# Kernel tuning notes

Measured on AMD Instinct MI355X. Metric: run time of the kernel, lower is better.

Reference implementation:

```python
import jax, jax.numpy as jnp
import numpy as np

B, S, D, H = 4, 2048, 1024, 16
DK = D // H

def setup_inputs() -> dict:
    key = jax.random.key(0)
    ks = jax.random.split(key, 12)
    s = 1.0 / np.sqrt(D)
    return {
        "query": jax.random.normal(ks[0], (B, S, D), jnp.float32),
        "key": jax.random.normal(ks[1], (B, S, D), jnp.float32),
        "value": jax.random.normal(ks[2], (B, S, D), jnp.float32),
        "mask": jax.random.randint(ks[3], (B, S, S), 0, 2, jnp.int32),
        "Wq": jax.random.normal(ks[4], (D, D), jnp.float32) * s,
        "bq": jnp.zeros((D,), jnp.float32),
        "Wk": jax.random.normal(ks[5], (D, D), jnp.float32) * s,
        "bk": jnp.zeros((D,), jnp.float32),
        "Wv": jax.random.normal(ks[6], (D, D), jnp.float32) * s,
        "bv": jnp.zeros((D,), jnp.float32),
        "Wo": jax.random.normal(ks[7], (D, D), jnp.float32) * s,
        "bo": jnp.zeros((D,), jnp.float32),
    }

def _split_heads(x):
    b, s, _ = x.shape
    return x.reshape(b, s, H, DK).transpose(0, 2, 1, 3)  # [b,h,s,dk]

def reference(query, key, value, mask, Wq, bq, Wk, bk, Wv, bv, Wo, bo):
    # torch nn.Linear: y = x @ W.T + b
    Q = _split_heads(query @ Wq.T + bq)
    K = _split_heads(key @ Wk.T + bk)
    V = _split_heads(value @ Wv.T + bv)
    scores = jnp.einsum('bhqd,bhkd->bhqk', Q, K) / np.sqrt(DK)
    scores = jnp.where(mask[:, None, :, :] == 0, jnp.float32(-1e9), scores)
    probs = jax.nn.softmax(scores, axis=-1)
    attn = jnp.einsum('bhqk,bhkd->bhqd', probs, V)
    out = attn.transpose(0, 2, 1, 3).reshape(query.shape[0], -1, H * DK)
    return out @ Wo.T + bo
```

## Files before the change

kernel.cpp:

```cpp
#include <hip/hip_runtime.h>

typedef __attribute__((ext_vector_type(8))) short short8;
typedef __attribute__((ext_vector_type(8))) unsigned short ushort8_t;
typedef __attribute__((ext_vector_type(4))) float floatx4;
typedef __attribute__((ext_vector_type(2))) _Float16 half2_t;
typedef __attribute__((ext_vector_type(4))) _Float16 half4;
typedef __attribute__((ext_vector_type(8))) _Float16 half8;
typedef __attribute__((ext_vector_type(2))) unsigned int uint2v;

#define B_ 4
#define S_ 2048
#define D_ 1024
#define H_ 16
#define DK_ 64
#define BS_ (B_ * S_)

union V8u { half8 v8; half4 v4[2]; };
union H16 { _Float16 h; unsigned short u; };

typedef const __attribute__((address_space(1))) void* gvp;
typedef __attribute__((address_space(3))) void* lvp;

static __device__ __forceinline__ unsigned short f2bf(float f) {
  union { float f; unsigned int u; } x; x.f = f;
  unsigned int r = x.u + 0x7fffu + ((x.u >> 16) & 1u);
  return (unsigned short)(r >> 16);
}

static __device__ __forceinline__ half2_t pk_f16(float a, float b) {
  return __builtin_bit_cast(half2_t, __builtin_amdgcn_cvt_pkrtz(a, b));
}

static __device__ __forceinline__ float fexp2(float x) {
  float r;
  asm("v_exp_f32 %0, %1" : "=v"(r) : "v"(x));
  return r;
}

static __device__ __forceinline__ half8 mk8(uint2v a, uint2v b) {
  union { unsigned u[4]; half8 h; } t;
  t.u[0] = a.x; t.u[1] = a.y; t.u[2] = b.x; t.u[3] = b.y;
  return t.h;
}

__global__ void cast3_kernel(const float* __restrict__ a, const float* __restrict__ b,
                             const float* __restrict__ c,
                             unsigned short* __restrict__ oa, unsigned short* __restrict__ ob,
                             unsigned short* __restrict__ oc, int n4) {
  int i = blockIdx.x * blockDim.x + threadIdx.x;
  int w = blockIdx.y;
  const float* src = (w == 0) ? a : (w == 1) ? b : c;
  unsigned short* dst = (w == 0) ? oa : (w == 1) ? ob : oc;
  if (i < n4) {
    float4 v = ((const float4*)src)[i];
    ushort4 o;
    o.x = f2bf(v.x); o.y = f2bf(v.y); o.z = f2bf(v.z); o.w = f2bf(v.w);
    ((ushort4*)dst)[i] = o;
  }
}

__global__ void cast4_kernel(const float* __restrict__ a, const float* __restrict__ b,
                             const float* __restrict__ c, const float* __restrict__ d,
                             unsigned short* __restrict__ oa, unsigned short* __restrict__ ob,
                             unsigned short* __restrict__ oc, unsigned short* __restrict__ od, int n4) {
  int i = blockIdx.x * blockDim.x + threadIdx.x;
  int w = blockIdx.y;
  const float* src = (w == 0) ? a : (w == 1) ? b : (w == 2) ? c : d;
  unsigned short* dst = (w == 0) ? oa : (w == 1) ? ob : (w == 2) ? oc : od;
  if (i < n4) {
    float4 v = ((const float4*)src)[i];
    ushort4 o;
    o.x = f2bf(v.x); o.y = f2bf(v.y); o.z = f2bf(v.z); o.w = f2bf(v.w);
    ((ushort4*)dst)[i] = o;
  }
}

__global__ void pack_mask(const int* __restrict__ mask, unsigned long long* __restrict__ bits) {
  int i = blockIdx.x * blockDim.x + threadIdx.x;
  unsigned long long m = __ballot(mask[i] != 0);
  if ((threadIdx.x & 63) == 0) bits[i >> 6] = m;
}

__global__ void transpose_v(const unsigned short* __restrict__ Vh, unsigned short* __restrict__ Vt) {
  __shared__ unsigned short T[64][72];
  int bh = blockIdx.y;
  int s0 = blockIdx.x * 64;
  int tid = threadIdx.x;
  int r = tid >> 3, c = (tid & 7) * 8;
  const unsigned short* src = Vh + ((size_t)bh * S_ + s0) * DK_;
#pragma unroll
  for (int p = 0; p < 2; ++p)
    *(uint4*)(&T[r + p * 32][c]) = *(const uint4*)(src + (size_t)(r + p * 32) * DK_ + c);
  __syncthreads();
  unsigned short* dst = Vt + (size_t)bh * DK_ * S_;
#pragma unroll
  for (int p = 0; p < 2; ++p) {
    int d = r + p * 32;
    ushort8_t o;
#pragma unroll
    for (int i = 0; i < 8; ++i) {
      int pos = c + i;
      int th = pos >> 5, rem = pos & 31;
      int q4 = rem >> 3, rem2 = rem & 7;
      int t = th * 2 + (rem2 >> 2), j = rem2 & 3;
      int k = t * 16 + q4 * 4 + j;
      o[i] = T[k][d];
    }
    *(ushort8_t*)(dst + (size_t)d * S_ + s0 + c) = o;
  }
}

__device__ __forceinline__ void gemm_core(
    const unsigned short* __restrict__ X, const unsigned short* __restrict__ W,
    const float* __restrict__ bias, void* __restrict__ Y,
    float scale, int mode, int bm, int bn,
    unsigned short* As, unsigned short* Bs)
{
  constexpr int K = D_, N = D_;
  int tid = threadIdx.x;
  int wave = tid >> 6, lane = tid & 63, quad = lane >> 4, li = lane & 15;
  int wm = wave >> 1, wn = wave & 1;
  int srow = lane >> 3;
  int scol = ((lane & 7) ^ srow) * 8;
  const unsigned short* gA = X + (size_t)(bm * 128 + wave * 32 + srow) * K + scol;
  const unsigned short* gB = W + (size_t)(bn * 128 + wave * 32 + srow) * K + scol;

  auto stage = [&](int buf, int k0) {
#pragma unroll
    for (int j = 0; j < 4; ++j) {
      __builtin_amdgcn_global_load_lds((gvp)(gA + (size_t)(j * 8) * K + k0),
          (lvp)(As + buf * 8192 + wave * 2048 + j * 512), 16, 0, 0);
      __builtin_amdgcn_global_load_lds((gvp)(gB + (size_t)(j * 8) * K + k0),
          (lvp)(Bs + buf * 8192 + wave * 2048 + j * 512), 16, 0, 0);
    }
  };

  floatx4 acc[4][4] = {};
  stage(0, 0);
  constexpr int NK = K / 64;
  for (int i = 0; i < NK; ++i) {
    int buf = i & 1;
    __syncthreads();
    if (i + 1 < NK) stage(buf ^ 1, (i + 1) * 64);
    short8 af[2][4], bf[2][4];
#pragma unroll
    for (int s2 = 0; s2 < 2; ++s2)
#pragma unroll
      for (int t = 0; t < 4; ++t) {
        int slot = ((s2 * 4 + quad) ^ (li & 7)) * 8;
        af[s2][t] = *(const short8*)(&As[buf * 8192 + (wm * 64 + t * 16 + li) * 64 + slot]);
        bf[s2][t] = *(const short8*)(&Bs[buf * 8192 + (wn * 64 + t * 16 + li) * 64 + slot]);
      }
#pragma unroll
    for (int s2 = 0; s2 < 2; ++s2)
#pragma unroll
      for (int mt = 0; mt < 4; ++mt)
#pragma unroll
        for (int nt = 0; nt < 4; ++nt)
          acc[mt][nt] = __builtin_amdgcn_mfma_f32_16x16x32_bf16(af[s2][mt], bf[s2][nt], acc[mt][nt], 0, 0, 0);
  }

#pragma unroll
  for (int nt = 0; nt < 4; ++nt) {
    int n = bn * 128 + wn * 64 + nt * 16 + li;
    float bv = bias[n];
#pragma unroll
    for (int mt = 0; mt < 4; ++mt) {
#pragma unroll
      for (int r = 0; r < 4; ++r) {
        int m = bm * 128 + wm * 64 + mt * 16 + quad * 4 + r;
        float v = (acc[mt][nt][r] + bv) * scale;
        if (mode == 1) {
          ((float*)Y)[(size_t)m * N + n] = v;
        } else {
          int b = m >> 11, s = m & 2047, h = n >> 6, dk = n & 63;
          size_t idx = (((size_t)(b * H_ + h)) * S_ + s) * DK_ + dk;
          if (mode == 0) {
            ((unsigned short*)Y)[idx] = f2bf(v);
          } else {
            H16 hv; hv.h = (_Float16)v;
            ((unsigned short*)Y)[idx] = hv.u;
          }
        }
      }
    }
  }
}

__global__ __launch_bounds__(256) void gemm_qkv(
    const unsigned short* __restrict__ Xq, const unsigned short* __restrict__ Xk,
    const unsigned short* __restrict__ Xv,
    const unsigned short* __restrict__ Wq, const unsigned short* __restrict__ Wk,
    const unsigned short* __restrict__ Wv,
    const float* __restrict__ bq, const float* __restrict__ bk, const float* __restrict__ bv,
    unsigned short* __restrict__ Qh, unsigned short* __restrict__ Kh,
    unsigned short* __restrict__ Vh, float sc)
{
  __shared__ __align__(16) unsigned short As[2 * 8192];
  __shared__ __align__(16) unsigned short Bs[2 * 8192];
  int z = blockIdx.z;
  const unsigned short* X = (z == 0) ? Xq : (z == 1) ? Xk : Xv;
  const unsigned short* W = (z == 0) ? Wq : (z == 1) ? Wk : Wv;
  const float* bias = (z == 0) ? bq : (z == 1) ? bk : bv;
  void* Y = (z == 0) ? (void*)Qh : (z == 1) ? (void*)Kh : (void*)Vh;
  float scale = (z == 0) ? sc : 1.0f;
  int mode = (z == 2) ? 2 : 0;
  gemm_core(X, W, bias, Y, scale, mode, blockIdx.y, blockIdx.x, As, Bs);
}

__global__ __launch_bounds__(256) void gemm_out(
    const unsigned short* __restrict__ X, const unsigned short* __restrict__ W,
    const float* __restrict__ bias, float* __restrict__ Y)
{
  __shared__ __align__(16) unsigned short As[2 * 8192];
  __shared__ __align__(16) unsigned short Bs[2 * 8192];
  gemm_core(X, W, bias, Y, 1.0f, 1, blockIdx.y, blockIdx.x, As, Bs);
}

__global__ __launch_bounds__(256) void attn_kernel(
    const unsigned short* __restrict__ Qh,
    const unsigned short* __restrict__ Kh,
    const _Float16* __restrict__ Vt,
    const unsigned long long* __restrict__ mbits,
    unsigned short* __restrict__ attnb)
{
  __shared__ __align__(16) unsigned short Ks[2 * 4096];
  __shared__ __align__(16) unsigned short Vs[2 * 4096];
  __shared__ __align__(8) uint2v mlut[16];

  int tid = threadIdx.x;
  int wave = tid >> 6, lane = tid & 63, quad = lane >> 4, li = lane & 15;

  if (tid < 16) {
    unsigned nb = (unsigned)tid;
    uint2v m;
    m.x = (nb & 1u ? 0x0000FFFFu : 0u) | (nb & 2u ? 0xFFFF0000u : 0u);
    m.y = (nb & 4u ? 0x0000FFFFu : 0u) | (nb & 8u ? 0xFFFF0000u : 0u);
    mlut[tid] = m;
  }

  int blk = blockIdx.x;
  int xcd = blk & 7, slot7 = blk >> 3;
  int bh = xcd * 8 + (slot7 >> 4);
  int qb = slot7 & 15;
  int b = bh >> 4, h = bh & 15;
  int qbase = qb * 128 + wave * 32;
  const size_t hq = (size_t)bh * S_ * DK_;

  short8 aQ[2][2];
#pragma unroll
  for (int qs = 0; qs < 2; ++qs)
#pragma unroll
    for (int s2 = 0; s2 < 2; ++s2)
      aQ[qs][s2] = *(const short8*)(Qh + hq + (size_t)(qbase + qs * 16 + li) * DK_ + s2 * 32 + quad * 8);

  floatx4 o[2][4] = {};
  floatx4 lacc[2] = {};
  const half8 ones8 = {(_Float16)1.f, (_Float16)1.f, (_Float16)1.f, (_Float16)1.f,
                       (_Float16)1.f, (_Float16)1.f, (_Float16)1.f, (_Float16)1.f};

  const unsigned long long* mrow = mbits + ((size_t)b * S_ + qbase + li) * (S_ / 64);

  int srow = lane >> 3;
  int scol = ((lane & 7) ^ srow) * 8;
  const unsigned short* gK = Kh + hq + (size_t)(wave * 16 + srow) * DK_ + scol;
  const _Float16* gV = Vt + ((size_t)bh * 64 + wave * 16 + srow) * S_ + scol;

  auto stage = [&](int buf, int k0) {
#pragma unroll
    for (int j = 0; j < 2; ++j) {
      __builtin_amdgcn_global_load_lds((gvp)(gK + (size_t)(k0 + j * 8) * DK_),
          (lvp)(Ks + buf * 4096 + wave * 1024 + j * 512), 16, 0, 0);
      __builtin_amdgcn_global_load_lds((gvp)(gV + (size_t)(j * 8) * S_ + k0),
          (lvp)(Vs + buf * 4096 + wave * 1024 + j * 512), 16, 0, 0);
    }
  };

  stage(0, 0);
  unsigned long long mw0c = mrow[0];
  unsigned long long mw1c = mrow[16 * (S_ / 64)];

  constexpr int NK = S_ / 64;
#pragma unroll 2
  for (int i = 0; i < NK; ++i) {
    int buf = i & 1;
    __syncthreads();
    if (i + 1 < NK) stage(buf ^ 1, (i + 1) * 64);
    unsigned long long mw0n = 0, mw1n = 0;
    if (i + 1 < NK) { mw0n = mrow[i + 1]; mw1n = mrow[16 * (S_ / 64) + i + 1]; }

    short8 bK[4][2];
#pragma unroll
    for (int t = 0; t < 4; ++t)
#pragma unroll
      for (int s2 = 0; s2 < 2; ++s2)
        bK[t][s2] = *(const short8*)(&Ks[buf * 4096 + (t * 16 + li) * 64 + (((s2 * 4 + quad) ^ (li & 7)) * 8)]);

    V8u vv[4][2];
#pragma unroll
    for (int dt = 0; dt < 4; ++dt)
#pragma unroll
      for (int tp = 0; tp < 2; ++tp)
        vv[dt][tp].v8 = *(const half8*)((const _Float16*)&Vs[buf * 4096 + (dt * 16 + li) * 64 + (((tp * 4 + quad) ^ (li & 7)) * 8)]);

    floatx4 sc[4][2] = {};
    __builtin_amdgcn_s_setprio(1);
#pragma unroll
    for (int s2 = 0; s2 < 2; ++s2)
#pragma unroll
      for (int t = 0; t < 4; ++t)
#pragma unroll
        for (int qs = 0; qs < 2; ++qs)
          sc[t][qs] = __builtin_amdgcn_mfma_f32_16x16x32_bf16(bK[t][s2], aQ[qs][s2], sc[t][qs], 0, 0, 0);
    __builtin_amdgcn_s_setprio(0);

    unsigned long long sh0 = mw0c >> (quad * 4);
    unsigned long long sh1 = mw1c >> (quad * 4);

    uint2v aPu[4][2];
#pragma unroll
    for (int t = 0; t < 4; ++t)
#pragma unroll
      for (int qs = 0; qs < 2; ++qs) {
        unsigned nb = (unsigned)(((qs ? sh1 : sh0) >> (t * 16)) & 15u);
        uint2v mm = mlut[nb];
        float p0 = fexp2(sc[t][qs][0]);
        float p1 = fexp2(sc[t][qs][1]);
        float p2 = fexp2(sc[t][qs][2]);
        float p3 = fexp2(sc[t][qs][3]);
        uint2v pp;
        pp.x = __builtin_bit_cast(unsigned, pk_f16(p0, p1)) & mm.x;
        pp.y = __builtin_bit_cast(unsigned, pk_f16(p2, p3)) & mm.y;
        aPu[t][qs] = pp;
      }

    __builtin_amdgcn_s_setprio(1);
#pragma unroll
    for (int a = 0; a < 2; ++a)
#pragma unroll
      for (int qs = 0; qs < 2; ++qs) {
        half8 pa = mk8(aPu[2 * a][qs], aPu[2 * a + 1][qs]);
        lacc[qs] = __builtin_amdgcn_mfma_f32_16x16x32_f16(pa, ones8, lacc[qs], 0, 0, 0);
#pragma unroll
        for (int dt = 0; dt < 4; ++dt)
          o[qs][dt] = __builtin_amdgcn_mfma_f32_16x16x32_f16(pa, vv[dt][a].v8, o[qs][dt], 0, 0, 0);
      }
    __builtin_amdgcn_s_setprio(0);

    mw0c = mw0n; mw1c = mw1n;
  }

#pragma unroll
  for (int qs = 0; qs < 2; ++qs)
#pragma unroll
    for (int r = 0; r < 4; ++r) {
      float ir = 1.0f / lacc[qs][r];
      size_t row = (size_t)b * S_ + qbase + qs * 16 + quad * 4 + r;
#pragma unroll
      for (int dt = 0; dt < 4; ++dt)
        attnb[row * D_ + h * DK_ + dt * 16 + li] = f2bf(o[qs][dt][r] * ir);
    }
}

extern "C" void kernel_launch(void* const* d_in, const int* in_sizes, int n_in,
                              void* d_out, int out_size, void* d_ws, size_t ws_size,
                              hipStream_t stream) {
  const float* query = (const float*)d_in[0];
  const float* key   = (const float*)d_in[1];
  const float* value = (const float*)d_in[2];
  const int*   mask  = (const int*)d_in[3];
  const float* Wq = (const float*)d_in[4];
  const float* bq = (const float*)d_in[5];
  const float* Wk = (const float*)d_in[6];
  const float* bk = (const float*)d_in[7];
  const float* Wv = (const float*)d_in[8];
  const float* bv = (const float*)d_in[9];
  const float* Wo = (const float*)d_in[10];
  const float* bo = (const float*)d_in[11];
  float* out = (float*)d_out;

  char* ws = (char*)d_ws;
  size_t off = 0;
  auto alloc = [&](size_t bytes) -> void* {
    void* p = ws + off;
    off += (bytes + 255) & ~(size_t)255;
    return p;
  };
  unsigned short* Xq    = (unsigned short*)alloc((size_t)BS_ * D_ * 2);
  unsigned short* Xk    = (unsigned short*)alloc((size_t)BS_ * D_ * 2);
  unsigned short* Xv    = (unsigned short*)alloc((size_t)BS_ * D_ * 2);
  unsigned short* Wqb   = (unsigned short*)alloc((size_t)D_ * D_ * 2);
  unsigned short* Wkb   = (unsigned short*)alloc((size_t)D_ * D_ * 2);
  unsigned short* Wvb   = (unsigned short*)alloc((size_t)D_ * D_ * 2);
  unsigned short* Wob   = (unsigned short*)alloc((size_t)D_ * D_ * 2);
  unsigned short* Qh    = (unsigned short*)alloc((size_t)BS_ * D_ * 2);
  unsigned short* Kh    = (unsigned short*)alloc((size_t)BS_ * D_ * 2);
  unsigned short* Vh    = (unsigned short*)alloc((size_t)BS_ * D_ * 2);
  unsigned short* Vt    = (unsigned short*)alloc((size_t)BS_ * D_ * 2);
  unsigned short* attnb = (unsigned short*)alloc((size_t)BS_ * D_ * 2);
  unsigned long long* mbits = (unsigned long long*)alloc((size_t)B_ * S_ * (S_ / 64) * 8);

  const float SC = 0.18033688011112042f;

  pack_mask<<<(B_ * S_ * S_) / 256, 256, 0, stream>>>(mask, mbits);

  int wn4 = D_ * D_ / 4;
  cast4_kernel<<<dim3(wn4 / 256, 4), 256, 0, stream>>>(Wq, Wk, Wv, Wo, Wqb, Wkb, Wvb, Wob, wn4);

  int xn4 = BS_ * D_ / 4;
  cast3_kernel<<<dim3(xn4 / 256, 3), 256, 0, stream>>>(query, key, value, Xq, Xk, Xv, xn4);

  gemm_qkv<<<dim3(D_ / 128, BS_ / 128, 3), 256, 0, stream>>>(
      Xq, Xk, Xv, Wqb, Wkb, Wvb, bq, bk, bv, Qh, Kh, Vh, SC);

  transpose_v<<<dim3(S_ / 64, B_ * H_), 256, 0, stream>>>(Vh, Vt);

  attn_kernel<<<dim3(8 * 8 * 16), 256, 0, stream>>>(Qh, Kh, (const _Float16*)Vt, mbits, attnb);

  gemm_out<<<dim3(D_ / 128, BS_ / 128), 256, 0, stream>>>(attnb, Wob, bo, out);
}
```

Measured before the change: 442.3 us.

## Triple-buffer K/V tiles and widen attention blocks to 8 waves

The attention kernel now runs 512 threads per block, so each block covers 256 queries instead of 128. This halves the K/V tile loads per query. K/V staging moves from double to triple buffering. The old __syncthreads is replaced by a manual vmcnt wait plus a single barrier per iteration, which lets the load for tile i+2 overlap compute on tile i. The risks are a fragile wait count that depends on how many global loads are outstanding, fewer blocks in the grid, and register pressure under the new launch bounds.

Measured after the change: 796.0 us. 80.0% more time.

```diff
diff --git a/kernel.cpp b/kernel.cpp
--- a/kernel.cpp
+++ b/kernel.cpp
@@ -217,34 +217,34 @@
   gemm_core(X, W, bias, Y, 1.0f, 1, blockIdx.y, blockIdx.x, As, Bs);
 }
 
-__global__ __launch_bounds__(256) void attn_kernel(
+__global__ __launch_bounds__(512, 4) void attn_kernel(
     const unsigned short* __restrict__ Qh,
     const unsigned short* __restrict__ Kh,
     const _Float16* __restrict__ Vt,
     const unsigned long long* __restrict__ mbits,
     unsigned short* __restrict__ attnb)
 {
-  __shared__ __align__(16) unsigned short Ks[2 * 4096];
-  __shared__ __align__(16) unsigned short Vs[2 * 4096];
+  __shared__ __align__(16) unsigned short Ks[3 * 4096];
+  __shared__ __align__(16) unsigned short Vs[3 * 4096];
   __shared__ __align__(8) uint2v mlut[16];
 
   int tid = threadIdx.x;
   int wave = tid >> 6, lane = tid & 63, quad = lane >> 4, li = lane & 15;
 
-  if (tid < 16) {
-    unsigned nb = (unsigned)tid;
+  if (lane < 16) {
+    unsigned nb = (unsigned)lane;
     uint2v m;
     m.x = (nb & 1u ? 0x0000FFFFu : 0u) | (nb & 2u ? 0xFFFF0000u : 0u);
     m.y = (nb & 4u ? 0x0000FFFFu : 0u) | (nb & 8u ? 0xFFFF0000u : 0u);
-    mlut[tid] = m;
+    mlut[nb] = m;
   }
 
   int blk = blockIdx.x;
-  int xcd = blk & 7, slot7 = blk >> 3;
-  int bh = xcd * 8 + (slot7 >> 4);
-  int qb = slot7 & 15;
+  int xcd = blk & 7, slot = blk >> 3;
+  int bh = xcd * 8 + (slot >> 3);
+  int qb = slot & 7;
   int b = bh >> 4, h = bh & 15;
-  int qbase = qb * 128 + wave * 32;
+  int qbase = qb * 256 + wave * 32;
   const size_t hq = (size_t)bh * S_ * DK_;
 
   short8 aQ[2][2];
@@ -263,29 +263,30 @@
 
   int srow = lane >> 3;
   int scol = ((lane & 7) ^ srow) * 8;
-  const unsigned short* gK = Kh + hq + (size_t)(wave * 16 + srow) * DK_ + scol;
-  const _Float16* gV = Vt + ((size_t)bh * 64 + wave * 16 + srow) * S_ + scol;
-
-  auto stage = [&](int buf, int k0) {
-#pragma unroll
-    for (int j = 0; j < 2; ++j) {
-      __builtin_amdgcn_global_load_lds((gvp)(gK + (size_t)(k0 + j * 8) * DK_),
-          (lvp)(Ks + buf * 4096 + wave * 1024 + j * 512), 16, 0, 0);
-      __builtin_amdgcn_global_load_lds((gvp)(gV + (size_t)(j * 8) * S_ + k0),
-          (lvp)(Vs + buf * 4096 + wave * 1024 + j * 512), 16, 0, 0);
-    }
+  const unsigned short* gK = Kh + hq + (size_t)(wave * 8 + srow) * DK_ + scol;
+  const _Float16* gV = Vt + ((size_t)bh * 64 + wave * 8 + srow) * S_ + scol;
+
+  auto stage = [&](int o3, int kb) {
+    __builtin_amdgcn_global_load_lds((gvp)(gK + (size_t)(kb * 64) * DK_),
+        (lvp)(Ks + o3 + wave * 512), 16, 0, 0);
+    __builtin_amdgcn_global_load_lds((gvp)(gV + (size_t)(kb * 64)),
+        (lvp)(Vs + o3 + wave * 512), 16, 0, 0);
   };
 
   stage(0, 0);
+  stage(4096, 1);
   unsigned long long mw0c = mrow[0];
   unsigned long long mw1c = mrow[16 * (S_ / 64)];
 
+  int o0 = 0, o1 = 4096, o2 = 8192;
+
   constexpr int NK = S_ / 64;
-#pragma unroll 2
   for (int i = 0; i < NK; ++i) {
-    int buf = i & 1;
-    __syncthreads();
-    if (i + 1 < NK) stage(buf ^ 1, (i + 1) * 64);
+    asm volatile("s_waitcnt vmcnt(4)" ::: "memory");
+    __builtin_amdgcn_s_barrier();
+    __builtin_amdgcn_sched_barrier(0);
+
+    if (i + 2 < NK) stage(o2, i + 2);
     unsigned long long mw0n = 0, mw1n = 0;
     if (i + 1 < NK) { mw0n = mrow[i + 1]; mw1n = mrow[16 * (S_ / 64) + i + 1]; }
 
@@ -294,14 +295,14 @@
     for (int t = 0; t < 4; ++t)
 #pragma unroll
       for (int s2 = 0; s2 < 2; ++s2)
-        bK[t][s2] = *(const short8*)(&Ks[buf * 4096 + (t * 16 + li) * 64 + (((s2 * 4 + quad) ^ (li & 7)) * 8)]);
+        bK[t][s2] = *(const short8*)(&Ks[o0 + (t * 16 + li) * 64 + (((s2 * 4 + quad) ^ (li & 7)) * 8)]);
 
     V8u vv[4][2];
 #pragma unroll
     for (int dt = 0; dt < 4; ++dt)
 #pragma unroll
       for (int tp = 0; tp < 2; ++tp)
-        vv[dt][tp].v8 = *(const half8*)((const _Float16*)&Vs[buf * 4096 + (dt * 16 + li) * 64 + (((tp * 4 + quad) ^ (li & 7)) * 8)]);
+        vv[dt][tp].v8 = *(const half8*)((const _Float16*)&Vs[o0 + (dt * 16 + li) * 64 + (((tp * 4 + quad) ^ (li & 7)) * 8)]);
 
     floatx4 sc[4][2] = {};
     __builtin_amdgcn_s_setprio(1);
@@ -348,6 +349,7 @@
     __builtin_amdgcn_s_setprio(0);
 
     mw0c = mw0n; mw1c = mw1n;
+    int tb = o0; o0 = o1; o1 = o2; o2 = tb;
   }
 
 #pragma unroll
@@ -415,7 +417,7 @@
 
   transpose_v<<<dim3(S_ / 64, B_ * H_), 256, 0, stream>>>(Vh, Vt);
 
-  attn_kernel<<<dim3(8 * 8 * 16), 256, 0, stream>>>(Qh, Kh, (const _Float16*)Vt, mbits, attnb);
+  attn_kernel<<<dim3(512), 512, 0, stream>>>(Qh, Kh, (const _Float16*)Vt, mbits, attnb);
 
   gemm_out<<<dim3(D_ / 128, BS_ / 128), 256, 0, stream>>>(attnb, Wob, bo, out);
 }
```

## Fuse V transpose into QKV GEMM epilogue and merge cast kernels

Applied to the files above, without the earlier changes.

The V projection epilogue now writes fp16 output directly in the transposed, permuted layout the attention kernel expects, which removes the separate transpose_v kernel and the Vh intermediate buffer. The three-input and four-weight cast kernels are merged into one launch. Together these remove a full read/write pass over V and one or two kernel launches. The risk is that the packed 8-byte stores strided along S in the GEMM epilogue coalesce less well than the old layout, and the permutation must exactly match the old transpose mapping.

New measurement: 415.2 us. 6.1% less time.

```diff
diff --git a/kernel.cpp b/kernel.cpp
--- a/kernel.cpp
+++ b/kernel.cpp
@@ -14,6 +14,8 @@
 #define H_ 16
 #define DK_ 64
 #define BS_ (B_ * S_)
+#define XN4_ (BS_ * D_ / 4)
+#define WN4_ (D_ * D_ / 4)
 
 union V8u { half8 v8; half4 v4[2]; };
 union H16 { _Float16 h; unsigned short u; };
@@ -43,71 +45,36 @@
   return t.h;
 }
 
-__global__ void cast3_kernel(const float* __restrict__ a, const float* __restrict__ b,
-                             const float* __restrict__ c,
-                             unsigned short* __restrict__ oa, unsigned short* __restrict__ ob,
-                             unsigned short* __restrict__ oc, int n4) {
+__global__ void cast_all(const float* __restrict__ q, const float* __restrict__ k,
+                         const float* __restrict__ v,
+                         const float* __restrict__ wq, const float* __restrict__ wk,
+                         const float* __restrict__ wv, const float* __restrict__ wo,
+                         unsigned short* __restrict__ oq, unsigned short* __restrict__ ok,
+                         unsigned short* __restrict__ ov,
+                         unsigned short* __restrict__ owq, unsigned short* __restrict__ owk,
+                         unsigned short* __restrict__ owv, unsigned short* __restrict__ owo) {
   int i = blockIdx.x * blockDim.x + threadIdx.x;
-  int w = blockIdx.y;
-  const float* src = (w == 0) ? a : (w == 1) ? b : c;
-  unsigned short* dst = (w == 0) ? oa : (w == 1) ? ob : oc;
-  if (i < n4) {
-    float4 v = ((const float4*)src)[i];
-    ushort4 o;
-    o.x = f2bf(v.x); o.y = f2bf(v.y); o.z = f2bf(v.z); o.w = f2bf(v.w);
-    ((ushort4*)dst)[i] = o;
-  }
-}
-
-__global__ void cast4_kernel(const float* __restrict__ a, const float* __restrict__ b,
-                             const float* __restrict__ c, const float* __restrict__ d,
-                             unsigned short* __restrict__ oa, unsigned short* __restrict__ ob,
-                             unsigned short* __restrict__ oc, unsigned short* __restrict__ od, int n4) {
-  int i = blockIdx.x * blockDim.x + threadIdx.x;
-  int w = blockIdx.y;
-  const float* src = (w == 0) ? a : (w == 1) ? b : (w == 2) ? c : d;
-  unsigned short* dst = (w == 0) ? oa : (w == 1) ? ob : (w == 2) ? oc : od;
-  if (i < n4) {
-    float4 v = ((const float4*)src)[i];
-    ushort4 o;
-    o.x = f2bf(v.x); o.y = f2bf(v.y); o.z = f2bf(v.z); o.w = f2bf(v.w);
-    ((ushort4*)dst)[i] = o;
-  }
+  const float* src; unsigned short* dst; int j;
+  if (i < 3 * XN4_) {
+    int w = i >> 21; j = i & (XN4_ - 1);
+    src = (w == 0) ? q : (w == 1) ? k : v;
+    dst = (w == 0) ? oq : (w == 1) ? ok : ov;
+  } else {
+    int t = i - 3 * XN4_;
+    int w = t >> 18; j = t & (WN4_ - 1);
+    src = (w == 0) ? wq : (w == 1) ? wk : (w == 2) ? wv : wo;
+    dst = (w == 0) ? owq : (w == 1) ? owk : (w == 2) ? owv : owo;
+  }
+  float4 v4 = ((const float4*)src)[j];
+  ushort4 o;
+  o.x = f2bf(v4.x); o.y = f2bf(v4.y); o.z = f2bf(v4.z); o.w = f2bf(v4.w);
+  ((ushort4*)dst)[j] = o;
 }
 
 __global__ void pack_mask(const int* __restrict__ mask, unsigned long long* __restrict__ bits) {
   int i = blockIdx.x * blockDim.x + threadIdx.x;
   unsigned long long m = __ballot(mask[i] != 0);
   if ((threadIdx.x & 63) == 0) bits[i >> 6] = m;
-}
-
-__global__ void transpose_v(const unsigned short* __restrict__ Vh, unsigned short* __restrict__ Vt) {
-  __shared__ unsigned short T[64][72];
-  int bh = blockIdx.y;
-  int s0 = blockIdx.x * 64;
-  int tid = threadIdx.x;
-  int r = tid >> 3, c = (tid & 7) * 8;
-  const unsigned short* src = Vh + ((size_t)bh * S_ + s0) * DK_;
-#pragma unroll
-  for (int p = 0; p < 2; ++p)
-    *(uint4*)(&T[r + p * 32][c]) = *(const uint4*)(src + (size_t)(r + p * 32) * DK_ + c);
-  __syncthreads();
-  unsigned short* dst = Vt + (size_t)bh * DK_ * S_;
-#pragma unroll
-  for (int p = 0; p < 2; ++p) {
-    int d = r + p * 32;
-    ushort8_t o;
-#pragma unroll
-    for (int i = 0; i < 8; ++i) {
-      int pos = c + i;
-      int th = pos >> 5, rem = pos & 31;
-      int q4 = rem >> 3, rem2 = rem & 7;
-      int t = th * 2 + (rem2 >> 2), j = rem2 & 3;
-      int k = t * 16 + q4 * 4 + j;
-      o[i] = T[k][d];
-    }
-    *(ushort8_t*)(dst + (size_t)d * S_ + s0 + c) = o;
-  }
 }
 
 __device__ __forceinline__ void gemm_core(
@@ -160,6 +127,33 @@
           acc[mt][nt] = __builtin_amdgcn_mfma_f32_16x16x32_bf16(af[s2][mt], bf[s2][nt], acc[mt][nt], 0, 0, 0);
   }
 
+  if (mode == 3) {
+    int mbase = bm * 128 + wm * 64;
+    int b0 = mbase >> 11;
+    int sblk = mbase & 2047;
+#pragma unroll
+    for (int nt = 0; nt < 4; ++nt) {
+      int n = bn * 128 + wn * 64 + nt * 16 + li;
+      float bv = bias[n];
+      int h = n >> 6, dk = n & 63;
+#pragma unroll
+      for (int mt = 0; mt < 4; ++mt) {
+        int pos = (mt >> 1) * 32 + quad * 8 + (mt & 1) * 4;
+        H16 h0, h1, h2, h3;
+        h0.h = (_Float16)(acc[mt][nt][0] + bv);
+        h1.h = (_Float16)(acc[mt][nt][1] + bv);
+        h2.h = (_Float16)(acc[mt][nt][2] + bv);
+        h3.h = (_Float16)(acc[mt][nt][3] + bv);
+        uint2v pk;
+        pk.x = (unsigned)h0.u | ((unsigned)h1.u << 16);
+        pk.y = (unsigned)h2.u | ((unsigned)h3.u << 16);
+        size_t idx = (((size_t)(b0 * H_ + h)) * DK_ + dk) * S_ + sblk + pos;
+        *(uint2v*)((unsigned short*)Y + idx) = pk;
+      }
+    }
+    return;
+  }
+
 #pragma unroll
   for (int nt = 0; nt < 4; ++nt) {
     int n = bn * 128 + wn * 64 + nt * 16 + li;
@@ -175,12 +169,7 @@
         } else {
           int b = m >> 11, s = m & 2047, h = n >> 6, dk = n & 63;
           size_t idx = (((size_t)(b * H_ + h)) * S_ + s) * DK_ + dk;
-          if (mode == 0) {
-            ((unsigned short*)Y)[idx] = f2bf(v);
-          } else {
-            H16 hv; hv.h = (_Float16)v;
-            ((unsigned short*)Y)[idx] = hv.u;
-          }
+          ((unsigned short*)Y)[idx] = f2bf(v);
         }
       }
     }
@@ -194,7 +183,7 @@
     const unsigned short* __restrict__ Wv,
     const float* __restrict__ bq, const float* __restrict__ bk, const float* __restrict__ bv,
     unsigned short* __restrict__ Qh, unsigned short* __restrict__ Kh,
-    unsigned short* __restrict__ Vh, float sc)
+    unsigned short* __restrict__ Vt, float sc)
 {
   __shared__ __align__(16) unsigned short As[2 * 8192];
   __shared__ __align__(16) unsigned short Bs[2 * 8192];
@@ -202,9 +191,9 @@
   const unsigned short* X = (z == 0) ? Xq : (z == 1) ? Xk : Xv;
   const unsigned short* W = (z == 0) ? Wq : (z == 1) ? Wk : Wv;
   const float* bias = (z == 0) ? bq : (z == 1) ? bk : bv;
-  void* Y = (z == 0) ? (void*)Qh : (z == 1) ? (void*)Kh : (void*)Vh;
+  void* Y = (z == 0) ? (void*)Qh : (z == 1) ? (void*)Kh : (void*)Vt;
   float scale = (z == 0) ? sc : 1.0f;
-  int mode = (z == 2) ? 2 : 0;
+  int mode = (z == 2) ? 3 : 0;
   gemm_core(X, W, bias, Y, scale, mode, blockIdx.y, blockIdx.x, As, Bs);
 }
 
@@ -236,7 +225,7 @@
     uint2v m;
     m.x = (nb & 1u ? 0x0000FFFFu : 0u) | (nb & 2u ? 0xFFFF0000u : 0u);
     m.y = (nb & 4u ? 0x0000FFFFu : 0u) | (nb & 8u ? 0xFFFF0000u : 0u);
-    mlut[tid] = m;
+    mlut[nb] = m;
   }
 
   int blk = blockIdx.x;
@@ -395,7 +384,6 @@
   unsigned short* Wob   = (unsigned short*)alloc((size_t)D_ * D_ * 2);
   unsigned short* Qh    = (unsigned short*)alloc((size_t)BS_ * D_ * 2);
   unsigned short* Kh    = (unsigned short*)alloc((size_t)BS_ * D_ * 2);
-  unsigned short* Vh    = (unsigned short*)alloc((size_t)BS_ * D_ * 2);
   unsigned short* Vt    = (unsigned short*)alloc((size_t)BS_ * D_ * 2);
   unsigned short* attnb = (unsigned short*)alloc((size_t)BS_ * D_ * 2);
   unsigned long long* mbits = (unsigned long long*)alloc((size_t)B_ * S_ * (S_ / 64) * 8);
@@ -404,16 +392,12 @@
 
   pack_mask<<<(B_ * S_ * S_) / 256, 256, 0, stream>>>(mask, mbits);
 
-  int wn4 = D_ * D_ / 4;
-  cast4_kernel<<<dim3(wn4 / 256, 4), 256, 0, stream>>>(Wq, Wk, Wv, Wo, Wqb, Wkb, Wvb, Wob, wn4);
-
-  int xn4 = BS_ * D_ / 4;
-  cast3_kernel<<<dim3(xn4 / 256, 3), 256, 0, stream>>>(query, key, value, Xq, Xk, Xv, xn4);
+  cast_all<<<(3 * XN4_ + 4 * WN4_) / 256, 256, 0, stream>>>(
+      query, key, value, Wq, Wk, Wv, Wo,
+      Xq, Xk, Xv, Wqb, Wkb, Wvb, Wob);
 
   gemm_qkv<<<dim3(D_ / 128, BS_ / 128, 3), 256, 0, stream>>>(
-      Xq, Xk, Xv, Wqb, Wkb, Wvb, bq, bk, bv, Qh, Kh, Vh, SC);
-
-  transpose_v<<<dim3(S_ / 64, B_ * H_), 256, 0, stream>>>(Vh, Vt);
+      Xq, Xk, Xv, Wqb, Wkb, Wvb, bq, bk, bv, Qh, Kh, Vt, SC);
 
   attn_kernel<<<dim3(8 * 8 * 16), 256, 0, stream>>>(Qh, Kh, (const _Float16*)Vt, mbits, attnb);
 
```
